# Performance work log

Hardware: AMD Instinct MI355X
Metric: run time of the kernel (lower is better)

## Reference

```python
import jax, jax.numpy as jnp
import numpy as np

B, T, F, H = 512, 512, 64, 64  # batch, time, input feat, hidden


def setup_inputs() -> dict:
    key = jax.random.key(0)
    k1, k2, k3, k4 = jax.random.split(key, 4)
    ins = jax.random.normal(k1, (B, T, F), jnp.float32)
    resets = jax.random.randint(k2, (B, T), 0, 2).astype(bool)
    # Flax LSTMCell: 4 input->hidden dense (no bias) + 4 hidden->hidden dense (bias),
    # concatenated here as [i, f, g, o] blocks of width H.
    si = 1.0 / np.sqrt(F)
    sh = 1.0 / np.sqrt(H)
    Wi = jax.random.uniform(k3, (F, 4 * H), jnp.float32, -si, si)
    Wh = jax.random.uniform(k4, (H, 4 * H), jnp.float32, -sh, sh)
    b = jnp.zeros((4 * H,), jnp.float32)
    return {"ins": ins, "resets": resets, "Wi": Wi, "Wh": Wh, "b": b}


def reference(ins, resets, Wi, Wh, b):
    Bn, Tn, _ = ins.shape
    Hn = Wh.shape[0]

    def step(carry, xt):
        c, h = carry
        x_t, r_t = xt  # x_t: [B, F], r_t: [B]
        m = r_t[:, None]
        c = jnp.where(m, 0.0, c)  # reset to initialize_carry (zeros)
        h = jnp.where(m, 0.0, h)
        z = x_t @ Wi + h @ Wh + b  # [B, 4H]
        i, f, g, o = jnp.split(z, 4, axis=-1)
        i = jax.nn.sigmoid(i)
        f = jax.nn.sigmoid(f)
        g = jnp.tanh(g)
        o = jax.nn.sigmoid(o)
        c_new = f * c + i * g
        h_new = o * jnp.tanh(c_new)
        return (c_new, h_new), h_new

    c0 = jnp.zeros((Bn, Hn), ins.dtype)
    h0 = jnp.zeros((Bn, Hn), ins.dtype)
    xs = (jnp.swapaxes(ins, 0, 1), jnp.swapaxes(resets, 0, 1))  # time-major
    _, ys = jax.lax.scan(step, (c0, h0), xs)
    return jnp.swapaxes(ys, 0, 1)  # [B, T, H]
```

## Files before the change

kernel.cpp:

```cpp
#include <hip/hip_runtime.h>


typedef __attribute__((ext_vector_type(8))) short short8;
typedef __attribute__((ext_vector_type(4))) float f32x4;

#define NB 512
#define NT 512
#define NF 64
#define NH 64
#define NG 256
#define TCHUNK 32

__device__ __forceinline__ float rcp_fast(float x) { return __builtin_amdgcn_rcpf(x); }
__device__ __forceinline__ float sig_fast(float x) { return rcp_fast(1.0f + __expf(-x)); }
__device__ __forceinline__ float tanh_fast(float x) {
    return 1.0f - 2.0f * rcp_fast(1.0f + __expf(2.0f * x));
}
__device__ __forceinline__ unsigned short f2bf(float x) {
    unsigned u = __float_as_uint(x);
    unsigned r = (u + 0x7FFFu + ((u >> 16) & 1u)) >> 16;
    return (unsigned short)r;
}

__global__ void detect_resets_dtype(const unsigned int* __restrict__ r, int n,
                                    int* __restrict__ flag) {
    int bits = 0;
    for (int i = blockIdx.x * blockDim.x + threadIdx.x; i < n;
         i += gridDim.x * blockDim.x) {
        unsigned v = r[i];
        if (v == 0x3F800000u) bits |= 2;
        else if (v != 0u && v != 1u) bits |= 4;
    }
    if (bits) atomicOr(flag, bits);
}

__device__ __forceinline__ int decode_mode(const int* flag) {
    int fl = *flag;
    if ((fl & 2) && !(fl & 4)) return 2;
    if (fl & 4) return 1;
    return 0;
}
__device__ __forceinline__ int load_rst(const void* resets, int mode, long idx) {
    if (mode == 1) return ((const unsigned char*)resets)[idx] != 0;
    if (mode == 2) return ((const float*)resets)[idx] != 0.0f;
    return ((const int*)resets)[idx] != 0;
}

template<int ZBF>
__global__ __launch_bounds__(256, 2)
void zgemm_kernel(const float* __restrict__ ins, const float* __restrict__ Wi,
                  const float* __restrict__ bias, void* __restrict__ Zv) {
    const int lane = threadIdx.x & 63;
    const int w    = threadIdx.x >> 6;
    const int l15  = lane & 15;
    const int l4   = lane >> 4;
    const long bt0 = (long)blockIdx.x * 64;
    const int pbase = w * 64;

    short8 afr[4][2];
    f32x4  binit[4];
#pragma unroll
    for (int pt = 0; pt < 4; ++pt) {
        const int prow = pbase + pt * 16 + l15;
        const int n = (prow & 3) * 64 + (prow >> 2);
#pragma unroll
        for (int kc = 0; kc < 2; ++kc) {
            short8 f;
#pragma unroll
            for (int e = 0; e < 8; ++e) {
                const int k = kc * 32 + l4 * 8 + e;
                f[e] = (short)f2bf(Wi[k * NG + n]);
            }
            afr[pt][kc] = f;
        }
        f32x4 bi;
#pragma unroll
        for (int r = 0; r < 4; ++r) {
            const int pr = pbase + pt * 16 + l4 * 4 + r;
            const int n2 = (pr & 3) * 64 + (pr >> 2);
            bi[r] = bias[n2];
        }
        binit[pt] = bi;
    }

#pragma unroll
    for (int tt = 0; tt < 4; ++tt) {
        const long bt = bt0 + tt * 16 + l15;
        short8 bfr[2];
#pragma unroll
        for (int kc = 0; kc < 2; ++kc) {
            const float4* xp = (const float4*)(ins + bt * NF + kc * 32 + l4 * 8);
            float4 v0 = xp[0];
            float4 v1 = xp[1];
            short8 f;
            f[0] = (short)f2bf(v0.x); f[1] = (short)f2bf(v0.y);
            f[2] = (short)f2bf(v0.z); f[3] = (short)f2bf(v0.w);
            f[4] = (short)f2bf(v1.x); f[5] = (short)f2bf(v1.y);
            f[6] = (short)f2bf(v1.z); f[7] = (short)f2bf(v1.w);
            bfr[kc] = f;
        }
#pragma unroll
        for (int pt = 0; pt < 4; ++pt) {
            f32x4 acc = binit[pt];
            acc = __builtin_amdgcn_mfma_f32_16x16x32_bf16(afr[pt][0], bfr[0], acc, 0, 0, 0);
            acc = __builtin_amdgcn_mfma_f32_16x16x32_bf16(afr[pt][1], bfr[1], acc, 0, 0, 0);
            const int p0 = pbase + pt * 16 + l4 * 4;
            if (ZBF) {
                unsigned lo = (unsigned)f2bf(acc[0]) | ((unsigned)f2bf(acc[1]) << 16);
                unsigned hi = (unsigned)f2bf(acc[2]) | ((unsigned)f2bf(acc[3]) << 16);
                uint2* dst = (uint2*)((unsigned short*)Zv + bt * NG + p0);
                *dst = make_uint2(lo, hi);
            } else {
                f32x4* dst = (f32x4*)((float*)Zv + bt * NG + p0);
                *dst = acc;
            }
        }
    }
}

template<int ZBF>
__global__ __launch_bounds__(64, 1)
void lstm_recur_kernel(const void* __restrict__ Zv, const void* __restrict__ resets,
                       const float* __restrict__ Wh, float* __restrict__ out,
                       const int* __restrict__ flag) {
    const int b = blockIdx.x;
    const int j = threadIdx.x;
    const int mode = decode_mode(flag);

    float whi[NF], whf[NF], whg[NF], who[NF];
#pragma unroll
    for (int k = 0; k < NF; ++k) {
        whi[k] = Wh[k * NG + j];
        whf[k] = Wh[k * NG + NH + j];
        whg[k] = Wh[k * NG + 2 * NH + j];
        who[k] = Wh[k * NG + 3 * NH + j];
    }

    float h = 0.0f, c = 0.0f;
    const long base = (long)b * NT;

    float z0, z1, z2, z3;
    {
        if (ZBF) {
            const uint2 zz = *(const uint2*)((const unsigned short*)Zv + base * NG + j * 4);
            z0 = __uint_as_float(zz.x << 16);
            z1 = __uint_as_float(zz.x & 0xFFFF0000u);
            z2 = __uint_as_float(zz.y << 16);
            z3 = __uint_as_float(zz.y & 0xFFFF0000u);
        } else {
            const f32x4 zz = *(const f32x4*)((const float*)Zv + base * NG + j * 4);
            z0 = zz[0]; z1 = zz[1]; z2 = zz[2]; z3 = zz[3];
        }
    }
    int rc = load_rst(resets, mode, base);

    for (int t = 0; t < NT; ++t) {
        const long tn = base + (t + 1 < NT ? t + 1 : NT - 1);
        float n0, n1, n2, n3;
        if (ZBF) {
            const uint2 zz = *(const uint2*)((const unsigned short*)Zv + tn * NG + j * 4);
            n0 = __uint_as_float(zz.x << 16);
            n1 = __uint_as_float(zz.x & 0xFFFF0000u);
            n2 = __uint_as_float(zz.y << 16);
            n3 = __uint_as_float(zz.y & 0xFFFF0000u);
        } else {
            const f32x4 zz = *(const f32x4*)((const float*)Zv + tn * NG + j * 4);
            n0 = zz[0]; n1 = zz[1]; n2 = zz[2]; n3 = zz[3];
        }
        const int rn = load_rst(resets, mode, tn);

        float zi = z0, zf = z1, zg = z2, zo = z3;
        if (!rc) {
#pragma unroll
            for (int k = 0; k < NF; ++k) {
                const float hk = __uint_as_float(
                    (unsigned)__builtin_amdgcn_readlane(__float_as_uint(h), k));
                zi = fmaf(hk, whi[k], zi);
                zf = fmaf(hk, whf[k], zf);
                zg = fmaf(hk, whg[k], zg);
                zo = fmaf(hk, who[k], zo);
            }
        }
        const float ig = sig_fast(zi);
        const float fg = sig_fast(zf);
        const float gg = tanh_fast(zg);
        const float og = sig_fast(zo);
        const float cm = rc ? 0.0f : c;
        c = fmaf(fg, cm, ig * gg);
        h = og * tanh_fast(c);
        out[(base + t) * NH + j] = h;

        z0 = n0; z1 = n1; z2 = n2; z3 = n3;
        rc = rn;
    }
}

__global__ __launch_bounds__(256, 2)
void lstm_scan_kernel(const float* __restrict__ ins, const void* __restrict__ resets,
                      const float* __restrict__ Wi, const float* __restrict__ Wh,
                      const float* __restrict__ bias, float* __restrict__ out,
                      const int* __restrict__ flag) {
    const int b = blockIdx.x;
    const int j = threadIdx.x;
    int mode = flag ? decode_mode(flag) : 0;

    float wi[NF], wh[NF];
#pragma unroll
    for (int k = 0; k < NF; ++k) {
        wi[k] = Wi[k * NG + j];
        wh[k] = Wh[k * NG + j];
    }
    const float bj = bias[j];

    __shared__ __align__(16) float xs[TCHUNK][NF];
    __shared__ int rs[TCHUNK];
    __shared__ __align__(16) float hbuf[2][NH];
    __shared__ float zbuf[NG];

    float c = 0.0f;
    if (j < NH) { hbuf[0][j] = 0.0f; hbuf[1][j] = 0.0f; }
    __syncthreads();

    int cur = 0;
    for (int t0 = 0; t0 < NT; t0 += TCHUNK) {
        {
            const float4* src = (const float4*)(ins + ((size_t)b * NT + t0) * NF);
            float4* dst = (float4*)&xs[0][0];
            dst[j] = src[j];
            dst[j + 256] = src[j + 256];
            if (j < TCHUNK) rs[j] = load_rst(resets, mode, (long)b * NT + t0 + j);
        }
        __syncthreads();

        for (int tt = 0; tt < TCHUNK; ++tt) {
            const int t = t0 + tt;
            const int rst = rs[tt];
            float accx = bj, acch = 0.0f;
            const float4* xv4 = (const float4*)&xs[tt][0];
#pragma unroll
            for (int k4 = 0; k4 < NF / 4; ++k4) {
                float4 xv = xv4[k4];
                accx = fmaf(xv.x, wi[4 * k4 + 0], accx);
                accx = fmaf(xv.y, wi[4 * k4 + 1], accx);
                accx = fmaf(xv.z, wi[4 * k4 + 2], accx);
                accx = fmaf(xv.w, wi[4 * k4 + 3], accx);
            }
            if (!rst) {
                const float4* hv4 = (const float4*)&hbuf[cur][0];
#pragma unroll
                for (int k4 = 0; k4 < NF / 4; ++k4) {
                    float4 hv = hv4[k4];
                    acch = fmaf(hv.x, wh[4 * k4 + 0], acch);
                    acch = fmaf(hv.y, wh[4 * k4 + 1], acch);
                    acch = fmaf(hv.z, wh[4 * k4 + 2], acch);
                    acch = fmaf(hv.w, wh[4 * k4 + 3], acch);
                }
            }
            zbuf[j] = accx + acch;
            __syncthreads();
            if (j < NH) {
                float zi = zbuf[j], zf = zbuf[j + NH], zg = zbuf[j + 2 * NH], zo = zbuf[j + 3 * NH];
                float ig = sig_fast(zi), fg = sig_fast(zf), gg = tanh_fast(zg), og = sig_fast(zo);
                float cc = rst ? 0.0f : c;
                cc = fg * cc + ig * gg;
                c = cc;
                float hh = og * tanh_fast(cc);
                hbuf[cur ^ 1][j] = hh;
                out[((size_t)b * NT + t) * NH + j] = hh;
            }
            __syncthreads();
            cur ^= 1;
        }
    }
}

extern "C" void kernel_launch(void* const* d_in, const int* in_sizes, int n_in,
                              void* d_out, int out_size, void* d_ws, size_t ws_size,
                              hipStream_t stream) {
    const float* ins    = (const float*)d_in[0];
    const void*  resets = d_in[1];
    const float* Wi     = (const float*)d_in[2];
    const float* Wh     = (const float*)d_in[3];
    const float* bias   = (const float*)d_in[4];
    float* out = (float*)d_out;

    const size_t ZF32  = (size_t)NB * NT * NG * 4;
    const size_t ZBF16 = ZF32 / 2;
    const int nBT = NB * NT;

    if (ws_size >= ZF32 + 64) {
        int* flag = (int*)((char*)d_ws + ZF32);
        hipMemsetAsync(flag, 0, sizeof(int), stream);
        detect_resets_dtype<<<256, 256, 0, stream>>>((const unsigned int*)resets, nBT, flag);
        zgemm_kernel<0><<<nBT / 64, 256, 0, stream>>>(ins, Wi, bias, d_ws);
        lstm_recur_kernel<0><<<NB, 64, 0, stream>>>(d_ws, resets, Wh, out, flag);
    } else if (ws_size >= ZBF16 + 64) {
        int* flag = (int*)((char*)d_ws + ZBF16);
        hipMemsetAsync(flag, 0, sizeof(int), stream);
        detect_resets_dtype<<<256, 256, 0, stream>>>((const unsigned int*)resets, nBT, flag);
        zgemm_kernel<1><<<nBT / 64, 256, 0, stream>>>(ins, Wi, bias, d_ws);
        lstm_recur_kernel<1><<<NB, 64, 0, stream>>>(d_ws, resets, Wh, out, flag);
    } else {
        int* flag = nullptr;
        if (d_ws && ws_size >= sizeof(int)) {
            flag = (int*)d_ws;
            hipMemsetAsync(flag, 0, sizeof(int), stream);
            detect_resets_dtype<<<256, 256, 0, stream>>>((const unsigned int*)resets, nBT, flag);
        }
        lstm_scan_kernel<<<NB, 256, 0, stream>>>(ins, resets, Wi, Wh, bias, out, flag);
    }
}
```

Measured before the change: 553.6 us.

## Split recurrence across 256 threads per sequence with LDS h exchange and bf16 Z

The recurrence kernel now uses 256 threads per batch row, one per gate column, each holding 64 Wh weights. The hidden state is exchanged through double-buffered shared memory, and gate pre-activations are gathered with a barrier every step. This replaces the old 64-thread design that did 256 FMAs per step per thread through readlane broadcasts. The input GEMM now stages x tiles in LDS, uses a plain gate-major column layout, and always writes bf16 Z, so the fp32 Z path is dropped. Z and reset values are prefetched 8 steps ahead. The cost is a __syncthreads per timestep plus bf16 rounding of Z even when workspace would allow fp32.

Measured after the change: 453.2 us. -18.1%, faster.

```diff
diff --git a/kernel.cpp b/kernel.cpp
--- a/kernel.cpp
+++ b/kernel.cpp
@@ -18,8 +18,10 @@
 }
 __device__ __forceinline__ unsigned short f2bf(float x) {
     unsigned u = __float_as_uint(x);
-    unsigned r = (u + 0x7FFFu + ((u >> 16) & 1u)) >> 16;
-    return (unsigned short)r;
+    return (unsigned short)((u + 0x7FFFu + ((u >> 16) & 1u)) >> 16);
+}
+__device__ __forceinline__ float bf2f(unsigned short s) {
+    return __uint_as_float(((unsigned)s) << 16);
 }
 
 __global__ void detect_resets_dtype(const unsigned int* __restrict__ r, int n,
@@ -33,7 +35,6 @@
     }
     if (bits) atomicOr(flag, bits);
 }
-
 __device__ __forceinline__ int decode_mode(const int* flag) {
     int fl = *flag;
     if ((fl & 2) && !(fl & 4)) return 2;
@@ -46,52 +47,56 @@
     return ((const int*)resets)[idx] != 0;
 }
 
-template<int ZBF>
 __global__ __launch_bounds__(256, 2)
-void zgemm_kernel(const float* __restrict__ ins, const float* __restrict__ Wi,
-                  const float* __restrict__ bias, void* __restrict__ Zv) {
-    const int lane = threadIdx.x & 63;
-    const int w    = threadIdx.x >> 6;
-    const int l15  = lane & 15;
-    const int l4   = lane >> 4;
+void zgemm2(const float* __restrict__ ins, const float* __restrict__ Wi,
+            const float* __restrict__ bias, unsigned short* __restrict__ Z) {
+    const int tid = threadIdx.x;
+    const int lane = tid & 63;
+    const int w = tid >> 6;
+    const int l15 = lane & 15, l4 = lane >> 4;
     const long bt0 = (long)blockIdx.x * 64;
-    const int pbase = w * 64;
+    const int nbase = w << 6;
+
+    __shared__ __align__(16) float xs[64][68];
+
+    {
+        const float4* src = (const float4*)(ins + bt0 * NF);
+#pragma unroll
+        for (int i = 0; i < 4; ++i) {
+            const int q = tid + 256 * i;
+            const int row = q >> 4, c4 = (q & 15) << 2;
+            *(float4*)&xs[row][c4] = src[q];
+        }
+    }
 
     short8 afr[4][2];
-    f32x4  binit[4];
+    f32x4 binit[4];
 #pragma unroll
     for (int pt = 0; pt < 4; ++pt) {
-        const int prow = pbase + pt * 16 + l15;
-        const int n = (prow & 3) * 64 + (prow >> 2);
+        const int n = nbase + pt * 16 + l15;
 #pragma unroll
         for (int kc = 0; kc < 2; ++kc) {
             short8 f;
 #pragma unroll
-            for (int e = 0; e < 8; ++e) {
-                const int k = kc * 32 + l4 * 8 + e;
-                f[e] = (short)f2bf(Wi[k * NG + n]);
-            }
+            for (int e = 0; e < 8; ++e)
+                f[e] = (short)f2bf(Wi[(kc * 32 + l4 * 8 + e) * NG + n]);
             afr[pt][kc] = f;
         }
         f32x4 bi;
 #pragma unroll
-        for (int r = 0; r < 4; ++r) {
-            const int pr = pbase + pt * 16 + l4 * 4 + r;
-            const int n2 = (pr & 3) * 64 + (pr >> 2);
-            bi[r] = bias[n2];
-        }
+        for (int r = 0; r < 4; ++r) bi[r] = bias[nbase + pt * 16 + l4 * 4 + r];
         binit[pt] = bi;
     }
+    __syncthreads();
 
 #pragma unroll
     for (int tt = 0; tt < 4; ++tt) {
-        const long bt = bt0 + tt * 16 + l15;
         short8 bfr[2];
 #pragma unroll
         for (int kc = 0; kc < 2; ++kc) {
-            const float4* xp = (const float4*)(ins + bt * NF + kc * 32 + l4 * 8);
-            float4 v0 = xp[0];
-            float4 v1 = xp[1];
+            const float* rp = &xs[tt * 16 + l15][kc * 32 + l4 * 8];
+            const float4 v0 = *(const float4*)rp;
+            const float4 v1 = *(const float4*)(rp + 4);
             short8 f;
             f[0] = (short)f2bf(v0.x); f[1] = (short)f2bf(v0.y);
             f[2] = (short)f2bf(v0.z); f[3] = (short)f2bf(v0.w);
@@ -99,100 +104,134 @@
             f[6] = (short)f2bf(v1.z); f[7] = (short)f2bf(v1.w);
             bfr[kc] = f;
         }
+        const long bt = bt0 + tt * 16 + l15;
 #pragma unroll
         for (int pt = 0; pt < 4; ++pt) {
             f32x4 acc = binit[pt];
             acc = __builtin_amdgcn_mfma_f32_16x16x32_bf16(afr[pt][0], bfr[0], acc, 0, 0, 0);
             acc = __builtin_amdgcn_mfma_f32_16x16x32_bf16(afr[pt][1], bfr[1], acc, 0, 0, 0);
-            const int p0 = pbase + pt * 16 + l4 * 4;
-            if (ZBF) {
-                unsigned lo = (unsigned)f2bf(acc[0]) | ((unsigned)f2bf(acc[1]) << 16);
-                unsigned hi = (unsigned)f2bf(acc[2]) | ((unsigned)f2bf(acc[3]) << 16);
-                uint2* dst = (uint2*)((unsigned short*)Zv + bt * NG + p0);
-                *dst = make_uint2(lo, hi);
-            } else {
-                f32x4* dst = (f32x4*)((float*)Zv + bt * NG + p0);
-                *dst = acc;
-            }
-        }
-    }
-}
-
-template<int ZBF>
-__global__ __launch_bounds__(64, 1)
-void lstm_recur_kernel(const void* __restrict__ Zv, const void* __restrict__ resets,
-                       const float* __restrict__ Wh, float* __restrict__ out,
-                       const int* __restrict__ flag) {
+            unsigned lo = (unsigned)f2bf(acc[0]) | ((unsigned)f2bf(acc[1]) << 16);
+            unsigned hi = (unsigned)f2bf(acc[2]) | ((unsigned)f2bf(acc[3]) << 16);
+            *(uint2*)&Z[bt * NG + nbase + pt * 16 + l4 * 4] = make_uint2(lo, hi);
+        }
+    }
+}
+
+__global__ __launch_bounds__(256, 2)
+void lstm_recur2(const unsigned short* __restrict__ Z, const void* __restrict__ resets,
+                 const float* __restrict__ Wh, float* __restrict__ out,
+                 const int* __restrict__ flag) {
+    const int tid = threadIdx.x;
+    const int w = tid >> 6;
+    const int j = tid & 63;
+    const int p = (w << 6) + j;
     const int b = blockIdx.x;
-    const int j = threadIdx.x;
     const int mode = decode_mode(flag);
-
-    float whi[NF], whf[NF], whg[NF], who[NF];
-#pragma unroll
-    for (int k = 0; k < NF; ++k) {
-        whi[k] = Wh[k * NG + j];
-        whf[k] = Wh[k * NG + NH + j];
-        whg[k] = Wh[k * NG + 2 * NH + j];
-        who[k] = Wh[k * NG + 3 * NH + j];
-    }
-
-    float h = 0.0f, c = 0.0f;
     const long base = (long)b * NT;
 
-    float z0, z1, z2, z3;
-    {
-        if (ZBF) {
-            const uint2 zz = *(const uint2*)((const unsigned short*)Zv + base * NG + j * 4);
-            z0 = __uint_as_float(zz.x << 16);
-            z1 = __uint_as_float(zz.x & 0xFFFF0000u);
-            z2 = __uint_as_float(zz.y << 16);
-            z3 = __uint_as_float(zz.y & 0xFFFF0000u);
-        } else {
-            const f32x4 zz = *(const f32x4*)((const float*)Zv + base * NG + j * 4);
-            z0 = zz[0]; z1 = zz[1]; z2 = zz[2]; z3 = zz[3];
-        }
-    }
-    int rc = load_rst(resets, mode, base);
-
-    for (int t = 0; t < NT; ++t) {
-        const long tn = base + (t + 1 < NT ? t + 1 : NT - 1);
-        float n0, n1, n2, n3;
-        if (ZBF) {
-            const uint2 zz = *(const uint2*)((const unsigned short*)Zv + tn * NG + j * 4);
-            n0 = __uint_as_float(zz.x << 16);
-            n1 = __uint_as_float(zz.x & 0xFFFF0000u);
-            n2 = __uint_as_float(zz.y << 16);
-            n3 = __uint_as_float(zz.y & 0xFFFF0000u);
-        } else {
-            const f32x4 zz = *(const f32x4*)((const float*)Zv + tn * NG + j * 4);
-            n0 = zz[0]; n1 = zz[1]; n2 = zz[2]; n3 = zz[3];
-        }
-        const int rn = load_rst(resets, mode, tn);
-
-        float zi = z0, zf = z1, zg = z2, zo = z3;
-        if (!rc) {
-#pragma unroll
-            for (int k = 0; k < NF; ++k) {
-                const float hk = __uint_as_float(
-                    (unsigned)__builtin_amdgcn_readlane(__float_as_uint(h), k));
-                zi = fmaf(hk, whi[k], zi);
-                zf = fmaf(hk, whf[k], zf);
-                zg = fmaf(hk, whg[k], zg);
-                zo = fmaf(hk, who[k], zo);
-            }
-        }
-        const float ig = sig_fast(zi);
-        const float fg = sig_fast(zf);
-        const float gg = tanh_fast(zg);
-        const float og = sig_fast(zo);
-        const float cm = rc ? 0.0f : c;
-        c = fmaf(fg, cm, ig * gg);
-        h = og * tanh_fast(c);
-        out[(base + t) * NH + j] = h;
-
-        z0 = n0; z1 = n1; z2 = n2; z3 = n3;
-        rc = rn;
-    }
+    float wh[NF];
+#pragma unroll
+    for (int k = 0; k < NF; ++k) wh[k] = Wh[k * NG + p];
+
+    __shared__ float zx[2][NG];
+    __shared__ __align__(16) float hsh[4][2][NH];
+
+    hsh[w][0][j] = 0.0f;
+    __syncthreads();
+
+    float c = 0.0f;
+    int cb = 0;
+
+#define LCLAMP(T) (base + (((T) < NT - 1) ? (T) : (NT - 1)))
+
+    unsigned short zA0, zA1, zA2, zA3, zB0, zB1, zB2, zB3;
+    int rA0, rA1, rA2, rA3, rB0, rB1, rB2, rB3;
+    zA0 = Z[(base + 0) * NG + p]; zA1 = Z[(base + 1) * NG + p];
+    zA2 = Z[(base + 2) * NG + p]; zA3 = Z[(base + 3) * NG + p];
+    rA0 = load_rst(resets, mode, base + 0); rA1 = load_rst(resets, mode, base + 1);
+    rA2 = load_rst(resets, mode, base + 2); rA3 = load_rst(resets, mode, base + 3);
+    zB0 = Z[(base + 4) * NG + p]; zB1 = Z[(base + 5) * NG + p];
+    zB2 = Z[(base + 6) * NG + p]; zB3 = Z[(base + 7) * NG + p];
+    rB0 = load_rst(resets, mode, base + 4); rB1 = load_rst(resets, mode, base + 5);
+    rB2 = load_rst(resets, mode, base + 6); rB3 = load_rst(resets, mode, base + 7);
+
+#define STEP(T, ZPRE, RST) do {                                                \
+        float s = (ZPRE);                                                      \
+        if (!(RST)) {                                                          \
+            const f32x4* hp = (const f32x4*)&hsh[w][cb][0];                    \
+            float s0 = 0.f, s1 = 0.f, s2 = 0.f, s3 = 0.f;                      \
+            _Pragma("unroll")                                                  \
+            for (int k16 = 0; k16 < 4; ++k16) {                                \
+                const f32x4 ha = hp[k16 * 4 + 0];                              \
+                const f32x4 hb = hp[k16 * 4 + 1];                              \
+                const f32x4 hc = hp[k16 * 4 + 2];                              \
+                const f32x4 hd = hp[k16 * 4 + 3];                              \
+                s0 = fmaf(ha[0], wh[k16 * 16 + 0], s0);                        \
+                s0 = fmaf(ha[1], wh[k16 * 16 + 1], s0);                        \
+                s0 = fmaf(ha[2], wh[k16 * 16 + 2], s0);                        \
+                s0 = fmaf(ha[3], wh[k16 * 16 + 3], s0);                        \
+                s1 = fmaf(hb[0], wh[k16 * 16 + 4], s1);                        \
+                s1 = fmaf(hb[1], wh[k16 * 16 + 5], s1);                        \
+                s1 = fmaf(hb[2], wh[k16 * 16 + 6], s1);                        \
+                s1 = fmaf(hb[3], wh[k16 * 16 + 7], s1);                        \
+                s2 = fmaf(hc[0], wh[k16 * 16 + 8], s2);                        \
+                s2 = fmaf(hc[1], wh[k16 * 16 + 9], s2);                        \
+                s2 = fmaf(hc[2], wh[k16 * 16 + 10], s2);                       \
+                s2 = fmaf(hc[3], wh[k16 * 16 + 11], s2);                       \
+                s3 = fmaf(hd[0], wh[k16 * 16 + 12], s3);                       \
+                s3 = fmaf(hd[1], wh[k16 * 16 + 13], s3);                       \
+                s3 = fmaf(hd[2], wh[k16 * 16 + 14], s3);                       \
+                s3 = fmaf(hd[3], wh[k16 * 16 + 15], s3);                       \
+            }                                                                  \
+            s += (s0 + s1) + (s2 + s3);                                        \
+        }                                                                      \
+        zx[cb][p] = s;                                                         \
+        __syncthreads();                                                       \
+        const float zi = zx[cb][j];                                            \
+        const float zf = zx[cb][NH + j];                                       \
+        const float zg = zx[cb][2 * NH + j];                                   \
+        const float zo = zx[cb][3 * NH + j];                                   \
+        const float ig = sig_fast(zi);                                         \
+        const float fg = sig_fast(zf);                                         \
+        const float gg = tanh_fast(zg);                                        \
+        const float og = sig_fast(zo);                                         \
+        const float cm = (RST) ? 0.0f : c;                                     \
+        c = fmaf(fg, cm, ig * gg);                                             \
+        const float hv = og * tanh_fast(c);                                    \
+        hsh[w][cb ^ 1][j] = hv;                                                \
+        if (w == 0) out[(base + (T)) * NH + j] = hv;                           \
+        cb ^= 1;                                                               \
+    } while (0)
+
+    for (int t0 = 0; t0 < NT; t0 += 8) {
+        const float fA0 = bf2f(zA0), fA1 = bf2f(zA1), fA2 = bf2f(zA2), fA3 = bf2f(zA3);
+        const int qA0 = rA0, qA1 = rA1, qA2 = rA2, qA3 = rA3;
+        {
+            const long i0 = LCLAMP(t0 + 8), i1 = LCLAMP(t0 + 9);
+            const long i2 = LCLAMP(t0 + 10), i3 = LCLAMP(t0 + 11);
+            zA0 = Z[i0 * NG + p]; zA1 = Z[i1 * NG + p];
+            zA2 = Z[i2 * NG + p]; zA3 = Z[i3 * NG + p];
+            rA0 = load_rst(resets, mode, i0); rA1 = load_rst(resets, mode, i1);
+            rA2 = load_rst(resets, mode, i2); rA3 = load_rst(resets, mode, i3);
+        }
+        STEP(t0 + 0, fA0, qA0); STEP(t0 + 1, fA1, qA1);
+        STEP(t0 + 2, fA2, qA2); STEP(t0 + 3, fA3, qA3);
+
+        const float fB0 = bf2f(zB0), fB1 = bf2f(zB1), fB2 = bf2f(zB2), fB3 = bf2f(zB3);
+        const int qB0 = rB0, qB1 = rB1, qB2 = rB2, qB3 = rB3;
+        {
+            const long i0 = LCLAMP(t0 + 12), i1 = LCLAMP(t0 + 13);
+            const long i2 = LCLAMP(t0 + 14), i3 = LCLAMP(t0 + 15);
+            zB0 = Z[i0 * NG + p]; zB1 = Z[i1 * NG + p];
+            zB2 = Z[i2 * NG + p]; zB3 = Z[i3 * NG + p];
+            rB0 = load_rst(resets, mode, i0); rB1 = load_rst(resets, mode, i1);
+            rB2 = load_rst(resets, mode, i2); rB3 = load_rst(resets, mode, i3);
+        }
+        STEP(t0 + 4, fB0, qB0); STEP(t0 + 5, fB1, qB1);
+        STEP(t0 + 6, fB2, qB2); STEP(t0 + 7, fB3, qB3);
+    }
+#undef STEP
+#undef LCLAMP
 }
 
 __global__ __launch_bounds__(256, 2)
@@ -284,22 +323,15 @@
     const float* bias   = (const float*)d_in[4];
     float* out = (float*)d_out;
 
-    const size_t ZF32  = (size_t)NB * NT * NG * 4;
-    const size_t ZBF16 = ZF32 / 2;
+    const size_t ZBF16 = (size_t)NB * NT * NG * 2;
     const int nBT = NB * NT;
 
-    if (ws_size >= ZF32 + 64) {
-        int* flag = (int*)((char*)d_ws + ZF32);
-        hipMemsetAsync(flag, 0, sizeof(int), stream);
-        detect_resets_dtype<<<256, 256, 0, stream>>>((const unsigned int*)resets, nBT, flag);
-        zgemm_kernel<0><<<nBT / 64, 256, 0, stream>>>(ins, Wi, bias, d_ws);
-        lstm_recur_kernel<0><<<NB, 64, 0, stream>>>(d_ws, resets, Wh, out, flag);
-    } else if (ws_size >= ZBF16 + 64) {
+    if (ws_size >= ZBF16 + 64) {
         int* flag = (int*)((char*)d_ws + ZBF16);
         hipMemsetAsync(flag, 0, sizeof(int), stream);
         detect_resets_dtype<<<256, 256, 0, stream>>>((const unsigned int*)resets, nBT, flag);
-        zgemm_kernel<1><<<nBT / 64, 256, 0, stream>>>(ins, Wi, bias, d_ws);
-        lstm_recur_kernel<1><<<NB, 64, 0, stream>>>(d_ws, resets, Wh, out, flag);
+        zgemm2<<<nBT / 64, 256, 0, stream>>>(ins, Wi, bias, (unsigned short*)d_ws);
+        lstm_recur2<<<NB, 256, 0, stream>>>((const unsigned short*)d_ws, resets, Wh, out, flag);
     } else {
         int* flag = nullptr;
         if (d_ws && ws_size >= sizeof(int)) {
```
